# Kernel optimization log

Hardware: AMD Instinct MI355X
Metric: run time of the kernel (lower is better)

## Reference

```python
import jax, jax.numpy as jnp
import numpy as np

TAU_RA = 30.0
K3 = 2.0
DT = 0.1


def setup_inputs() -> dict:
    key = jax.random.key(0)
    I_in = jax.random.normal(key, (8, 4096, 2048), dtype=jnp.float32)
    return {"I_in": I_in}


def reference(I_in):
    # I_in: (batch, time, neurons)
    # finite-difference derivative; first step uses I_in[:,0]/dt
    dI = jnp.concatenate(
        [I_in[:, :1, :], I_in[:, 1:, :] - I_in[:, :-1, :]], axis=1
    ) / DT
    # drive term: k3*|dI|*dt/tau, decay a = 1 - dt/tau
    a = 1.0 - DT / TAU_RA
    drive = (K3 * DT / TAU_RA) * jnp.abs(dI)  # (B, T, N)
    # linear recurrence I_RA[t] = a * I_RA[t-1] + drive[t], I_RA[-1] = 0
    drive_t = jnp.swapaxes(drive, 0, 1)  # (T, B, N) for scan over time

    def step(state, u):
        new = a * state + u
        return new, new

    init = jnp.zeros(drive_t.shape[1:], dtype=I_in.dtype)
    _, outs = jax.lax.scan(step, init, drive_t)
    return jnp.swapaxes(outs, 0, 1)  # (B, T, N)
```

## Files before the change

### kernel.cpp

```cpp
#include <hip/hip_runtime.h>


constexpr int Bb  = 8;
constexpr int Tn  = 4096;
constexpr int Nn  = 2048;
constexpr int SEG = 16;
constexpr int L   = Tn / SEG;
constexpr int U   = 16;

__global__ __launch_bounds__(64 * SEG) void ra_filter2_kernel(
    const float* __restrict__ in, float* __restrict__ out) {
    const int lane = threadIdx.x & 63;
    const int s    = threadIdx.x >> 6;
    const int nb   = blockIdx.x & (Nn / 64 - 1);
    const int b    = blockIdx.x >> 5;
    const int n    = nb * 64 + lane;

    const float a = 0.99666666666666667f;
    const float c = 0.06666666666666667f;
    float A = a;
#pragma unroll
    for (int i = 0; i < 8; ++i) A = A * A;

    const size_t base = (size_t)b * Tn * Nn + n;
    const int t0 = s * L;
    const float* p = in  + base + (size_t)t0 * Nn;
    float*       q = out + base + (size_t)t0 * Nn;

    float E = 0.0f;
    if (s < SEG - 1) {
        float prev = (t0 == 0) ? 0.0f : p[-(ptrdiff_t)Nn];
        float st = 0.0f;
        float xa[U], xb[U];
#pragma unroll
        for (int u = 0; u < U; ++u) xa[u] = p[(size_t)u * Nn];
        for (int tt = 0; tt < L; tt += 2 * U) {
#pragma unroll
            for (int u = 0; u < U; ++u) xb[u] = p[(size_t)(tt + U + u) * Nn];
#pragma unroll
            for (int u = 0; u < U; ++u) {
                float x = xa[u];
                st = fmaf(a, st, c * fabsf(x - prev));
                prev = x;
            }
            if (tt + 2 * U < L) {
#pragma unroll
                for (int u = 0; u < U; ++u) xa[u] = p[(size_t)(tt + 2 * U + u) * Nn];
            }
#pragma unroll
            for (int u = 0; u < U; ++u) {
                float x = xb[u];
                st = fmaf(a, st, c * fabsf(x - prev));
                prev = x;
            }
        }
        E = st;
    }

    __shared__ float lds_E[SEG][64];
    lds_E[s][lane] = E;
    __syncthreads();

    float carry = 0.0f;
    for (int j = 0; j < s; ++j) carry = fmaf(A, carry, lds_E[j][lane]);

    {
        float prev = (t0 == 0) ? 0.0f : p[-(ptrdiff_t)Nn];
        float st = carry;
        float xa[U], xb[U];
#pragma unroll
        for (int u = 0; u < U; ++u) xa[u] = p[(size_t)u * Nn];
        for (int tt = 0; tt < L; tt += 2 * U) {
#pragma unroll
            for (int u = 0; u < U; ++u) xb[u] = p[(size_t)(tt + U + u) * Nn];
#pragma unroll
            for (int u = 0; u < U; ++u) {
                float x = xa[u];
                st = fmaf(a, st, c * fabsf(x - prev));
                prev = x;
                xa[u] = st;
            }
#pragma unroll
            for (int u = 0; u < U; ++u)
                __builtin_nontemporal_store(xa[u], q + (size_t)(tt + u) * Nn);
            if (tt + 2 * U < L) {
#pragma unroll
                for (int u = 0; u < U; ++u) xa[u] = p[(size_t)(tt + 2 * U + u) * Nn];
            }
#pragma unroll
            for (int u = 0; u < U; ++u) {
                float x = xb[u];
                st = fmaf(a, st, c * fabsf(x - prev));
                prev = x;
                xb[u] = st;
            }
#pragma unroll
            for (int u = 0; u < U; ++u)
                __builtin_nontemporal_store(xb[u], q + (size_t)(tt + U + u) * Nn);
        }
    }
}

extern "C" void kernel_launch(void* const* d_in, const int* in_sizes, int n_in,
                              void* d_out, int out_size, void* d_ws, size_t ws_size,
                              hipStream_t stream) {
    const float* in = (const float*)d_in[0];
    float* out = (float*)d_out;

    dim3 grid(Bb * (Nn / 64)), block(64 * SEG);
    hipLaunchKernelGGL(ra_filter2_kernel, grid, block, 0, stream, in, out);
}
```

Before: 465.3 us.

## Split time scan into two kernels with float4 columns and 64 segments

Replaces the single block-local two-phase scan with two kernel launches. The first kernel computes per-segment end states for 64 time segments and writes them to workspace. The second kernel combines prior segment states into a carry and rescans the segment to write outputs. Each thread now handles four neurons via float4 loads, and the decay power is adjusted for the shorter segments. The aim is more parallelism and wider memory accesses, at the cost of an extra launch, a global workspace round trip, and a carry loop that grows with segment index.

```diff
diff --git a/kernel.cpp b/kernel.cpp
--- a/kernel.cpp
+++ b/kernel.cpp
@@ -1,112 +1,143 @@
 #include <hip/hip_runtime.h>
 
 
-constexpr int Bb  = 8;
-constexpr int Tn  = 4096;
-constexpr int Nn  = 2048;
-constexpr int SEG = 16;
-constexpr int L   = Tn / SEG;
-constexpr int U   = 16;
+typedef float f4 __attribute__((ext_vector_type(4)));
 
-__global__ __launch_bounds__(64 * SEG) void ra_filter2_kernel(
-    const float* __restrict__ in, float* __restrict__ out) {
+constexpr int Bb   = 8;
+constexpr int Tn   = 4096;
+constexpr int Nn   = 2048;
+constexpr int NQ   = Nn / 4;
+constexpr int QTOT = Bb * NQ;
+constexpr int COLS = QTOT / 64;
+constexpr int SEG  = 64;
+constexpr int L    = Tn / SEG;
+constexpr int U    = 8;
+constexpr int WPB  = 8;
+
+__device__ __forceinline__ void step4(f4& st, f4& prev, const f4 x,
+                                      float a, float c) {
+#pragma unroll
+    for (int i = 0; i < 4; ++i)
+        st[i] = fmaf(a, st[i], c * fabsf(x[i] - prev[i]));
+    prev = x;
+}
+
+__global__ __launch_bounds__(64 * WPB) void ra_passA(
+    const f4* __restrict__ in4, f4* __restrict__ E4) {
     const int lane = threadIdx.x & 63;
-    const int s    = threadIdx.x >> 6;
-    const int nb   = blockIdx.x & (Nn / 64 - 1);
-    const int b    = blockIdx.x >> 5;
-    const int n    = nb * 64 + lane;
+    const int wid  = threadIdx.x >> 6;
+    const int seg  = blockIdx.x / (COLS / WPB);
+    const int col  = (blockIdx.x % (COLS / WPB)) * WPB + wid;
+    const int q    = col * 64 + lane;
+    const int b    = q >> 9;
+    const int nq   = q & (NQ - 1);
+    const int t0   = seg * L;
+
+    const float a = 0.99666666666666667f;
+    const float c = 0.06666666666666667f;
+
+    const f4* p = in4 + ((size_t)b * Tn + t0) * NQ + nq;
+
+    f4 prev = (t0 > 0) ? __builtin_nontemporal_load(p - NQ) : (f4)(0.f);
+    f4 st = (f4)(0.f);
+
+    f4 xa[U], xb[U];
+#pragma unroll
+    for (int u = 0; u < U; ++u)
+        xa[u] = __builtin_nontemporal_load(p + (size_t)u * NQ);
+
+    for (int tt = 0; tt < L; tt += 2 * U) {
+#pragma unroll
+        for (int u = 0; u < U; ++u)
+            xb[u] = __builtin_nontemporal_load(p + (size_t)(tt + U + u) * NQ);
+#pragma unroll
+        for (int u = 0; u < U; ++u) step4(st, prev, xa[u], a, c);
+        if (tt + 2 * U < L) {
+#pragma unroll
+            for (int u = 0; u < U; ++u)
+                xa[u] = __builtin_nontemporal_load(p + (size_t)(tt + 2 * U + u) * NQ);
+        }
+#pragma unroll
+        for (int u = 0; u < U; ++u) step4(st, prev, xb[u], a, c);
+    }
+
+    E4[(size_t)seg * QTOT + q] = st;
+}
+
+__global__ __launch_bounds__(64 * WPB) void ra_passB(
+    const f4* __restrict__ in4, const f4* __restrict__ E4,
+    f4* __restrict__ out4) {
+    const int lane = threadIdx.x & 63;
+    const int wid  = threadIdx.x >> 6;
+    const int seg  = blockIdx.x / (COLS / WPB);
+    const int col  = (blockIdx.x % (COLS / WPB)) * WPB + wid;
+    const int q    = col * 64 + lane;
+    const int b    = q >> 9;
+    const int nq   = q & (NQ - 1);
+    const int t0   = seg * L;
 
     const float a = 0.99666666666666667f;
     const float c = 0.06666666666666667f;
     float A = a;
 #pragma unroll
-    for (int i = 0; i < 8; ++i) A = A * A;
+    for (int i = 0; i < 6; ++i) A *= A;
 
-    const size_t base = (size_t)b * Tn * Nn + n;
-    const int t0 = s * L;
-    const float* p = in  + base + (size_t)t0 * Nn;
-    float*       q = out + base + (size_t)t0 * Nn;
-
-    float E = 0.0f;
-    if (s < SEG - 1) {
-        float prev = (t0 == 0) ? 0.0f : p[-(ptrdiff_t)Nn];
-        float st = 0.0f;
-        float xa[U], xb[U];
+    f4 carry = (f4)(0.f);
+    for (int j = 0; j < seg; ++j) {
+        f4 e = E4[(size_t)j * QTOT + q];
 #pragma unroll
-        for (int u = 0; u < U; ++u) xa[u] = p[(size_t)u * Nn];
-        for (int tt = 0; tt < L; tt += 2 * U) {
-#pragma unroll
-            for (int u = 0; u < U; ++u) xb[u] = p[(size_t)(tt + U + u) * Nn];
-#pragma unroll
-            for (int u = 0; u < U; ++u) {
-                float x = xa[u];
-                st = fmaf(a, st, c * fabsf(x - prev));
-                prev = x;
-            }
-            if (tt + 2 * U < L) {
-#pragma unroll
-                for (int u = 0; u < U; ++u) xa[u] = p[(size_t)(tt + 2 * U + u) * Nn];
-            }
-#pragma unroll
-            for (int u = 0; u < U; ++u) {
-                float x = xb[u];
-                st = fmaf(a, st, c * fabsf(x - prev));
-                prev = x;
-            }
-        }
-        E = st;
+        for (int i = 0; i < 4; ++i) carry[i] = fmaf(A, carry[i], e[i]);
     }
 
-    __shared__ float lds_E[SEG][64];
-    lds_E[s][lane] = E;
-    __syncthreads();
+    const f4* p = in4  + ((size_t)b * Tn + t0) * NQ + nq;
+    f4*       o = out4 + ((size_t)b * Tn + t0) * NQ + nq;
 
-    float carry = 0.0f;
-    for (int j = 0; j < s; ++j) carry = fmaf(A, carry, lds_E[j][lane]);
+    f4 prev = (t0 > 0) ? __builtin_nontemporal_load(p - NQ) : (f4)(0.f);
+    f4 st = carry;
 
-    {
-        float prev = (t0 == 0) ? 0.0f : p[-(ptrdiff_t)Nn];
-        float st = carry;
-        float xa[U], xb[U];
+    f4 xa[U], xb[U];
 #pragma unroll
-        for (int u = 0; u < U; ++u) xa[u] = p[(size_t)u * Nn];
-        for (int tt = 0; tt < L; tt += 2 * U) {
+    for (int u = 0; u < U; ++u)
+        xa[u] = __builtin_nontemporal_load(p + (size_t)u * NQ);
+
+    for (int tt = 0; tt < L; tt += 2 * U) {
 #pragma unroll
-            for (int u = 0; u < U; ++u) xb[u] = p[(size_t)(tt + U + u) * Nn];
+        for (int u = 0; u < U; ++u)
+            xb[u] = __builtin_nontemporal_load(p + (size_t)(tt + U + u) * NQ);
 #pragma unroll
-            for (int u = 0; u < U; ++u) {
-                float x = xa[u];
-                st = fmaf(a, st, c * fabsf(x - prev));
-                prev = x;
-                xa[u] = st;
-            }
+        for (int u = 0; u < U; ++u) {
+            step4(st, prev, xa[u], a, c);
+            xa[u] = st;
+        }
+#pragma unroll
+        for (int u = 0; u < U; ++u)
+            __builtin_nontemporal_store(xa[u], o + (size_t)(tt + u) * NQ);
+        if (tt + 2 * U < L) {
 #pragma unroll
             for (int u = 0; u < U; ++u)
-                __builtin_nontemporal_store(xa[u], q + (size_t)(tt + u) * Nn);
-            if (tt + 2 * U < L) {
+                xa[u] = __builtin_nontemporal_load(p + (size_t)(tt + 2 * U + u) * NQ);
+        }
 #pragma unroll
-                for (int u = 0; u < U; ++u) xa[u] = p[(size_t)(tt + 2 * U + u) * Nn];
-            }
+        for (int u = 0; u < U; ++u) {
+            step4(st, prev, xb[u], a, c);
+            xb[u] = st;
+        }
 #pragma unroll
-            for (int u = 0; u < U; ++u) {
-                float x = xb[u];
-                st = fmaf(a, st, c * fabsf(x - prev));
-                prev = x;
-                xb[u] = st;
-            }
-#pragma unroll
-            for (int u = 0; u < U; ++u)
-                __builtin_nontemporal_store(xb[u], q + (size_t)(tt + U + u) * Nn);
-        }
+        for (int u = 0; u < U; ++u)
+            __builtin_nontemporal_store(xb[u], o + (size_t)(tt + U + u) * NQ);
     }
 }
 
 extern "C" void kernel_launch(void* const* d_in, const int* in_sizes, int n_in,
                               void* d_out, int out_size, void* d_ws, size_t ws_size,
                               hipStream_t stream) {
-    const float* in = (const float*)d_in[0];
-    float* out = (float*)d_out;
+    const f4* in4 = (const f4*)d_in[0];
+    f4* out4 = (f4*)d_out;
+    f4* E4 = (f4*)d_ws;
 
-    dim3 grid(Bb * (Nn / 64)), block(64 * SEG);
-    hipLaunchKernelGGL(ra_filter2_kernel, grid, block, 0, stream, in, out);
+    dim3 block(64 * WPB);
+    dim3 gridA((SEG - 1) * (COLS / WPB));
+    dim3 gridB(SEG * (COLS / WPB));
+    hipLaunchKernelGGL(ra_passA, gridA, block, 0, stream, in4, E4);
+    hipLaunchKernelGGL(ra_passB, gridB, block, 0, stream, in4, E4, out4);
 }
```

After: 497.4 us. +6.9%, slower.
